# Kernel optimization log

Measured on AMD Instinct MI355X. Metric: run time of the kernel, lower is better.

Reference implementation:

```python
import jax, jax.numpy as jnp
import numpy as np

TEMPERATURE = 12.5   # init temperature
SINKHORN_EPS = 0.05  # entropic regularization replacing exact cv2.EMD LP solve
SINKHORN_ITERS = 100 # fixed iteration count (jit-friendly)


def _weight_vector(A, B):
    # A: [M,C,H,W], B: [N,C,H,W] -> [M, N, H*W]
    # matches: global-avg-pool B over HW, inner product over channels per spatial node of A
    Bp = B.mean(axis=(2, 3))                      # [N, C]
    comb = jnp.einsum('mchw,nc->mnhw', A, Bp)     # [M, N, H, W]
    comb = comb.reshape(A.shape[0], B.shape[0], -1)
    return jax.nn.relu(comb) + 0.001


def _center(x):
    # norm='center': subtract channel mean (dim 1)
    return x - x.mean(axis=1, keepdims=True)


def _similarity_map(support, query):
    # metric='cosine': sim[q, w, i, j] = cos(query[q,:,i], support[w,:,j]) over channels
    s = support.reshape(support.shape[0], support.shape[1], -1)  # [W, C, Ns]
    q = query.reshape(query.shape[0], query.shape[1], -1)        # [Q, C, Nq]
    s = s / jnp.maximum(jnp.linalg.norm(s, axis=1, keepdims=True), 1e-8)
    q = q / jnp.maximum(jnp.linalg.norm(q, axis=1, keepdims=True), 1e-8)
    return jnp.einsum('qci,wcj->qwij', q, s)                     # [Q, W, Nq, Ns]


def _sinkhorn_flow(cost, a, b, eps=SINKHORN_EPS, n_iters=SINKHORN_ITERS):
    # Batched entropic OT in log-space. cost: [..., n, m]; a: [..., n]; b: [..., m].
    log_a = jnp.log(a)
    log_b = jnp.log(b)
    logK = -cost / eps

    def body(_, uv):
        u, v = uv
        u = log_a - jax.nn.logsumexp(logK + v[..., None, :], axis=-1)
        v = log_b - jax.nn.logsumexp(logK + u[..., None], axis=-2)
        return (u, v)

    u0 = jnp.zeros_like(log_a)
    v0 = jnp.zeros_like(log_b)
    u, v = jax.lax.fori_loop(0, n_iters, body, (u0, v0))
    return jnp.exp(logK + u[..., None] + v[..., None, :])  # transport plan [..., n, m]


def setup_inputs() -> dict:
    key = jax.random.key(0)
    k1, k2 = jax.random.split(key)
    support = jax.random.normal(k1, (32, 512, 8, 8), dtype=jnp.float32)
    query = jax.random.normal(k2, (256, 512, 8, 8), dtype=jnp.float32)
    return {"support": support, "query": query}


def reference(support, query):
    # weight_1: [Q, W, N] (row/query-node marginals), weight_2: [W, Q, N] (col/support-node)
    w1 = _weight_vector(query, support)
    w2 = _weight_vector(support, query)

    s = _center(support)
    q = _center(query)
    sim = _similarity_map(s, q)  # [Q, W, N, N]

    num_node = w1.shape[-1]
    # opencv path: relu (no-op, already >0) + 1e-5, rescale so each marginal sums to num_node
    a = w1 + 1e-5
    a = a * (num_node / a.sum(-1, keepdims=True))              # [Q, W, N]
    b = jnp.transpose(w2, (1, 0, 2)) + 1e-5                    # weight_2[j, i] -> [Q, W, N]
    b = b * (num_node / b.sum(-1, keepdims=True))

    flow = _sinkhorn_flow(1.0 - sim, a, b)                     # [Q, W, N, N]
    flow = jax.lax.stop_gradient(flow)  # opencv flow is a non-differentiable constant

    logits = (sim * flow).sum((-1, -2)) * (TEMPERATURE / num_node)  # [Q, W]
    return logits
```

## Files before the change

### kernel.cpp

```cpp
#include <hip/hip_runtime.h>
#include <math.h>


#define DEV static __device__ __forceinline__

typedef _Float16 half8 __attribute__((ext_vector_type(8)));
typedef float floatx4 __attribute__((ext_vector_type(4)));

DEV float fast_rcp(float x) {
#if __has_builtin(__builtin_amdgcn_rcpf)
    return __builtin_amdgcn_rcpf(x);
#else
    return 1.0f / x;
#endif
}
DEV float fexp2(float x) {
#if __has_builtin(__builtin_amdgcn_exp2f)
    return __builtin_amdgcn_exp2f(x);
#else
    return exp2f(x);
#endif
}
DEV float flog2(float x) {
#if __has_builtin(__builtin_amdgcn_logf)
    return __builtin_amdgcn_logf(x);
#else
    return log2f(x);
#endif
}

#define K_SIM2M 28.853900817779268f
#define K_M2SIM 0.034657359027997264f
#define LDP 68
#define LDPH 72

__global__ void __launch_bounds__(1024, 1)
norm_kernel(const float* __restrict__ support, const float* __restrict__ query,
            _Float16* __restrict__ Vht, _Float16* __restrict__ Uht,
            float* __restrict__ BpT, float* __restrict__ QpT,
            float* __restrict__ muA, float* __restrict__ nrmA,
            float* __restrict__ Ssc) {
    __shared__ float red1[16][64];
    __shared__ float red2[16][64];
    __shared__ float muL[64], invL[64];
    __shared__ float tile[128][65];

    int sid = blockIdx.x;
    const float* src;
    _Float16* dst;
    float* poolT;
    int pstride, pidx;
    if (sid < 32) {
        src = support + (size_t)sid * 32768; dst = Vht + (size_t)sid * 32768;
        poolT = BpT; pstride = 32; pidx = sid;
    } else {
        src = query + (size_t)(sid - 32) * 32768; dst = Uht + (size_t)(sid - 32) * 32768;
        poolT = QpT; pstride = 256; pidx = sid - 32;
    }

    int node = threadIdx.x & 63;
    int cq   = threadIdx.x >> 6;

    float s1 = 0.f, s2 = 0.f;
#pragma unroll 8
    for (int j = 0; j < 32; ++j) {
        int c = cq * 32 + j;
        float x = src[c * 64 + node];
        s1 += x; s2 += x * x;
        float ps = x;
        ps += __shfl_xor(ps, 1);  ps += __shfl_xor(ps, 2);  ps += __shfl_xor(ps, 4);
        ps += __shfl_xor(ps, 8);  ps += __shfl_xor(ps, 16); ps += __shfl_xor(ps, 32);
        if (node == 0) poolT[(size_t)c * pstride + pidx] = ps * (1.0f / 64.0f);
    }
    red1[cq][node] = s1;
    red2[cq][node] = s2;
    __syncthreads();
    if (threadIdx.x < 64) {
        float t1 = 0.f, t2 = 0.f;
#pragma unroll
        for (int k = 0; k < 16; ++k) { t1 += red1[k][node]; t2 += red2[k][node]; }
        float mu  = t1 * (1.0f / 512.0f);
        float ss  = t2 - 512.0f * mu * mu;
        float nrm = fmaxf(sqrtf(fmaxf(ss, 0.0f)), 1e-8f);
        muL[node]  = mu;
        invL[node] = 1.0f / nrm;
        muA[sid * 64 + node]  = mu;
        nrmA[sid * 64 + node] = nrm;
        float sS = t1;
        sS += __shfl_xor(sS, 1);  sS += __shfl_xor(sS, 2);  sS += __shfl_xor(sS, 4);
        sS += __shfl_xor(sS, 8);  sS += __shfl_xor(sS, 16); sS += __shfl_xor(sS, 32);
        if (node == 0) Ssc[sid] = sS * (1.0f / 64.0f);
    }
    __syncthreads();

    float mu = muL[node], inv = invL[node];
    for (int ch = 0; ch < 4; ++ch) {
#pragma unroll
        for (int j = 0; j < 8; ++j) {
            int cl = cq * 8 + j;
            float x = src[(ch * 128 + cl) * 64 + node];
            tile[cl][node] = (x - mu) * inv;
        }
        __syncthreads();
        {
            int g    = threadIdx.x;
            int slot = g & 63;
            int t    = (g >> 6) & 3;
            int kkl  = g >> 8;
            int nd   = t * 16 + (slot & 15);
            int c8   = (kkl << 2) | (slot >> 4);
            half8 v;
#pragma unroll
            for (int i = 0; i < 8; ++i) v[i] = (_Float16)tile[c8 * 8 + i][nd];
            *(half8*)(dst + ((size_t)ch * 1024 + g) * 8) = v;
        }
        __syncthreads();
    }
}

__global__ void __launch_bounds__(256)
marg_kernel(const _Float16* __restrict__ Uht, const _Float16* __restrict__ Vht,
            const float* __restrict__ BpT, const float* __restrict__ QpT,
            const float* __restrict__ muA, const float* __restrict__ nrmA,
            const float* __restrict__ Ssc,
            float* __restrict__ a_out, float* __restrict__ b_out) {
    __shared__ __align__(16) float WL[512 * 32];
    __shared__ float Sl[32];
    int lane = threadIdx.x & 63;
    int kq   = threadIdx.x >> 6;

    const _Float16* src16;
    float mu, nrm;
    if (blockIdx.x < 256) {
        int q = (blockIdx.x & 7) * 32 + (blockIdx.x >> 3);
        for (int t = threadIdx.x; t < 4096; t += 256)
            ((float4*)WL)[t] = ((const float4*)BpT)[t];
        if (threadIdx.x < 32) Sl[threadIdx.x] = Ssc[threadIdx.x];
        src16 = Uht + (size_t)q * 32768;
        mu  = muA[(32 + q) * 64 + lane];
        nrm = nrmA[(32 + q) * 64 + lane];
    } else {
        int id = blockIdx.x - 256;
        int w = id >> 3, qg = id & 7;
        for (int t = threadIdx.x; t < 4096; t += 256) {
            int c = t >> 3, k = t & 7;
            ((float4*)WL)[t] = ((const float4*)(QpT + (size_t)c * 256 + qg * 32))[k];
        }
        if (threadIdx.x < 32) Sl[threadIdx.x] = Ssc[32 + qg * 32 + threadIdx.x];
        src16 = Vht + (size_t)w * 32768;
        mu  = muA[w * 64 + lane];
        nrm = nrmA[w * 64 + lane];
    }
    __syncthreads();

    int lbase = (lane >> 4) * 64 + (lane & 15);
    float acc[8] = {0, 0, 0, 0, 0, 0, 0, 0};
#pragma unroll 1
    for (int kk = 0; kk < 16; ++kk) {
#pragma unroll
        for (int hi = 0; hi < 4; ++hi) {
            half8 x8 = *(const half8*)(src16 +
                        ((size_t)(kk * 256 + lbase + (hi << 4)) * 8));
            int cb = kk * 32 + hi * 8;
#pragma unroll
            for (int j = 0; j < 8; ++j) {
                float xv = (float)x8[j];
                const float* wl = WL + (cb + j) * 32 + kq * 8;
                float4 b0 = *(const float4*)wl;
                float4 b1 = *(const float4*)(wl + 4);
                acc[0] = fmaf(xv, b0.x, acc[0]); acc[1] = fmaf(xv, b0.y, acc[1]);
                acc[2] = fmaf(xv, b0.z, acc[2]); acc[3] = fmaf(xv, b0.w, acc[3]);
                acc[4] = fmaf(xv, b1.x, acc[4]); acc[5] = fmaf(xv, b1.y, acc[5]);
                acc[6] = fmaf(xv, b1.z, acc[6]); acc[7] = fmaf(xv, b1.w, acc[7]);
            }
        }
    }
#pragma unroll
    for (int k = 0; k < 8; ++k) {
        float raw = fmaf(mu, Sl[kq * 8 + k], nrm * acc[k]);
        float v = fmaxf(raw, 0.0f) + 0.001f;
        v += 1e-5f;
        float s = v;
        s += __shfl_xor(s, 1);  s += __shfl_xor(s, 2);  s += __shfl_xor(s, 4);
        s += __shfl_xor(s, 8);  s += __shfl_xor(s, 16); s += __shfl_xor(s, 32);
        v = v * (64.0f / s);
        if (blockIdx.x < 256) {
            int q = (blockIdx.x & 7) * 32 + (blockIdx.x >> 3), w = kq * 8 + k;
            a_out[((size_t)q * 32 + w) * 64 + lane] = v;
        } else {
            int id = blockIdx.x - 256;
            int w = id >> 3, q = (id & 7) * 32 + kq * 8 + k;
            b_out[((size_t)w * 256 + q) * 64 + lane] = v;
        }
    }
}

__global__ void __launch_bounds__(256, 4)
emd_kernel(const _Float16* __restrict__ Uht, const _Float16* __restrict__ Vht,
           const float* __restrict__ a_arr, const float* __restrict__ b_arr,
           float* __restrict__ out) {
    __shared__ __align__(16) _Float16 T[4][64 * LDPH];

    int x    = blockIdx.x & 7;
    int i    = blockIdx.x >> 3;
    int w    = i & 31;
    int wave = threadIdx.x >> 6;
    int lane = threadIdx.x & 63;
    int q    = (x * 8 + (i >> 5)) * 4 + wave;
    int lo16 = lane & 15;
    int hi4  = lane >> 4;
    int ig   = lane >> 3;
    int jg   = lane & 7;

    floatx4 acc[4][4];
#pragma unroll
    for (int tm = 0; tm < 4; ++tm)
#pragma unroll
        for (int tn = 0; tn < 4; ++tn)
            acc[tm][tn] = (floatx4){0.f, 0.f, 0.f, 0.f};

    const _Float16* Abase = Uht + (size_t)q * 32768 + lane * 8;
    const _Float16* Bbase = Vht + (size_t)w * 32768 + lane * 8;
#pragma unroll 1
    for (int kk = 0; kk < 16; ++kk) {
        half8 bf[4];
#pragma unroll
        for (int t = 0; t < 4; ++t)
            bf[t] = *(const half8*)(Bbase + (size_t)(kk * 4 + t) * 512);
#pragma unroll
        for (int tm = 0; tm < 4; ++tm) {
            half8 af = *(const half8*)(Abase + (size_t)(kk * 4 + tm) * 512);
#pragma unroll
            for (int tn = 0; tn < 4; ++tn)
                acc[tm][tn] = __builtin_amdgcn_mfma_f32_16x16x32_f16(
                    af, bf[tn], acc[tm][tn], 0, 0, 0);
        }
    }

    float lmax = -2.0f;
#pragma unroll
    for (int tm = 0; tm < 4; ++tm)
#pragma unroll
        for (int tn = 0; tn < 4; ++tn)
#pragma unroll
            for (int r = 0; r < 4; ++r) lmax = fmaxf(lmax, acc[tm][tn][r]);
    lmax = fmaxf(lmax, __shfl_xor(lmax, 1));
    lmax = fmaxf(lmax, __shfl_xor(lmax, 2));
    lmax = fmaxf(lmax, __shfl_xor(lmax, 4));
    lmax = fmaxf(lmax, __shfl_xor(lmax, 8));
    lmax = fmaxf(lmax, __shfl_xor(lmax, 16));
    lmax = fmaxf(lmax, __shfl_xor(lmax, 32));
    float s0 = lmax;

    {
        _Float16* buf = T[wave];
#pragma unroll
        for (int tm = 0; tm < 4; ++tm)
#pragma unroll
            for (int tn = 0; tn < 4; ++tn)
#pragma unroll
                for (int r = 0; r < 4; ++r) {
                    int row = tm * 16 + hi4 * 4 + r;
                    int col = tn * 16 + lo16;
                    int sp  = (col & 7) ^ (row >> 3);
                    buf[row * LDPH + (col & ~7) + sp] =
                        (_Float16)fexp2((acc[tm][tn][r] - s0) * K_SIM2M);
                }
    }
    __syncthreads();
    float Mf[8][8];
    {
        const _Float16* buf = T[wave];
#pragma unroll
        for (int t = 0; t < 8; ++t) {
            half8 h = *(const half8*)(buf + (ig * 8 + (jg ^ t)) * LDPH + jg * 8);
#pragma unroll
            for (int c = 0; c < 8; ++c) Mf[t][c] = (float)h[c];
        }
    }

    int gp = q * 32 + w;
    float a_own = a_arr[(size_t)gp * 64 + ig * 8 + jg];
    float b_own = b_arr[((size_t)w * 256 + q) * 64 + jg * 8 + ig];

    float wvp[8];
#pragma unroll
    for (int s = 0; s < 8; ++s) wvp[s] = 1.0f;
    float q8[8];
    float w_prev = -1.f;

#pragma unroll 1
    for (int it = 0; it < 100; ++it) {
        float p[8];
#pragma unroll
        for (int t = 0; t < 8; ++t) {
            float s = Mf[t][0] * wvp[0];
#pragma unroll
            for (int c = 1; c < 8; ++c) s = fmaf(Mf[t][c], wvp[c], s);
            p[t] = s;
        }
        p[0] += __shfl_xor(p[4], 4); p[1] += __shfl_xor(p[5], 4);
        p[2] += __shfl_xor(p[6], 4); p[3] += __shfl_xor(p[7], 4);
        p[0] += __shfl_xor(p[2], 2); p[1] += __shfl_xor(p[3], 2);
        p[0] += __shfl_xor(p[1], 1);
        float z_own = a_own * fast_rcp(p[0]);
        q8[0] = z_own;
        q8[1] = __shfl_xor(q8[0], 1);
        q8[2] = __shfl_xor(q8[0], 2); q8[3] = __shfl_xor(q8[1], 2);
        q8[4] = __shfl_xor(q8[0], 4); q8[5] = __shfl_xor(q8[1], 4);
        q8[6] = __shfl_xor(q8[2], 4); q8[7] = __shfl_xor(q8[3], 4);
        float cp[8];
#pragma unroll
        for (int s = 0; s < 8; ++s) {
            float v = Mf[0][s] * q8[0];
#pragma unroll
            for (int t = 1; t < 8; ++t) v = fmaf(Mf[t][s], q8[t], v);
            cp[s] = v;
        }
        cp[0] += __shfl_xor(cp[4], 32); cp[1] += __shfl_xor(cp[5], 32);
        cp[2] += __shfl_xor(cp[6], 32); cp[3] += __shfl_xor(cp[7], 32);
        cp[0] += __shfl_xor(cp[2], 16); cp[1] += __shfl_xor(cp[3], 16);
        cp[0] += __shfl_xor(cp[1], 8);
        float w_own = b_own * fast_rcp(cp[0]);
        wvp[0] = w_own;
        wvp[1] = __shfl_xor(wvp[0], 8);
        wvp[2] = __shfl_xor(wvp[0], 16); wvp[3] = __shfl_xor(wvp[1], 16);
        wvp[4] = __shfl_xor(wvp[0], 32); wvp[5] = __shfl_xor(wvp[1], 32);
        wvp[6] = __shfl_xor(wvp[2], 32); wvp[7] = __shfl_xor(wvp[3], 32);
        bool same = fabsf(w_own - w_prev) <= 1e-5f * w_own;
        w_prev = w_own;
        if (__all(same)) break;
    }

    float s = 0.f;
#pragma unroll
    for (int t = 0; t < 8; ++t)
#pragma unroll
        for (int c = 0; c < 8; ++c) {
            float m    = fmaxf(Mf[t][c], 1e-30f);
            float sim  = fmaf(flog2(m), K_M2SIM, s0);
            float flow = q8[t] * m * wvp[c];
            s = fmaf(sim, flow, s);
        }
    s += __shfl_xor(s, 1);  s += __shfl_xor(s, 2);  s += __shfl_xor(s, 4);
    s += __shfl_xor(s, 8);  s += __shfl_xor(s, 16); s += __shfl_xor(s, 32);
    if (lane == 0) out[gp] = s * 0.1953125f;
}

extern "C" void kernel_launch(void* const* d_in, const int* in_sizes, int n_in,
                              void* d_out, int out_size, void* d_ws, size_t ws_size,
                              hipStream_t stream) {
    (void)in_sizes; (void)n_in; (void)out_size; (void)ws_size;
    const float* support = (const float*)d_in[0];
    const float* query   = (const float*)d_in[1];

    char* ws = (char*)d_ws;
    _Float16* Uht = (_Float16*)ws;
    _Float16* Vht = Uht + 8388608;
    float* BpT  = (float*)(Vht + 1048576);
    float* QpT  = BpT + 16384;
    float* aA   = QpT + 131072;
    float* bA   = aA + 524288;
    float* muA  = bA + 524288;
    float* nrmA = muA + 18432;
    float* Ssc  = nrmA + 18432;

    norm_kernel<<<288, 1024, 0, stream>>>(support, query, Vht, Uht, BpT, QpT,
                                          muA, nrmA, Ssc);
    marg_kernel<<<512, 256, 0, stream>>>(Uht, Vht, BpT, QpT, muA, nrmA, Ssc,
                                         aA, bA);
    emd_kernel<<<2048, 256, 0, stream>>>(Uht, Vht, aA, bA, (float*)d_out);
}
```

Measured before the change: 183.5 us.

## Fuse marginal weight computation into EMD kernel, drop separate marg kernel

Removes the standalone marg_kernel and computes the pooled-weight marginals inside emd_kernel. It accumulates dot products of the fp16 feature fragments already loaded for the MFMA similarity GEMM against the pooled vectors, then reduces them across lanes. The pooled arrays are stored row-major so each wave can read its own pool vector. The EMD block shrinks to 2 waves with 4096 blocks. This removes a kernel launch and the a/b round trip through global memory, at the cost of redundant FMA work per (q,w) pair and more register pressure in the main kernel.

```diff
diff --git a/kernel.cpp b/kernel.cpp
--- a/kernel.cpp
+++ b/kernel.cpp
@@ -31,13 +31,12 @@
 
 #define K_SIM2M 28.853900817779268f
 #define K_M2SIM 0.034657359027997264f
-#define LDP 68
 #define LDPH 72
 
 __global__ void __launch_bounds__(1024, 1)
 norm_kernel(const float* __restrict__ support, const float* __restrict__ query,
             _Float16* __restrict__ Vht, _Float16* __restrict__ Uht,
-            float* __restrict__ BpT, float* __restrict__ QpT,
+            float* __restrict__ Bp, float* __restrict__ Qp,
             float* __restrict__ muA, float* __restrict__ nrmA,
             float* __restrict__ Ssc) {
     __shared__ float red1[16][64];
@@ -49,13 +48,13 @@
     const float* src;
     _Float16* dst;
     float* poolT;
-    int pstride, pidx;
+    int pidx;
     if (sid < 32) {
         src = support + (size_t)sid * 32768; dst = Vht + (size_t)sid * 32768;
-        poolT = BpT; pstride = 32; pidx = sid;
+        poolT = Bp; pidx = sid;
     } else {
         src = query + (size_t)(sid - 32) * 32768; dst = Uht + (size_t)(sid - 32) * 32768;
-        poolT = QpT; pstride = 256; pidx = sid - 32;
+        poolT = Qp; pidx = sid - 32;
     }
 
     int node = threadIdx.x & 63;
@@ -70,7 +69,7 @@
         float ps = x;
         ps += __shfl_xor(ps, 1);  ps += __shfl_xor(ps, 2);  ps += __shfl_xor(ps, 4);
         ps += __shfl_xor(ps, 8);  ps += __shfl_xor(ps, 16); ps += __shfl_xor(ps, 32);
-        if (node == 0) poolT[(size_t)c * pstride + pidx] = ps * (1.0f / 64.0f);
+        if (node == 0) poolT[(size_t)pidx * 512 + c] = ps * (1.0f / 64.0f);
     }
     red1[cq][node] = s1;
     red2[cq][node] = s2;
@@ -118,95 +117,20 @@
     }
 }
 
-__global__ void __launch_bounds__(256)
-marg_kernel(const _Float16* __restrict__ Uht, const _Float16* __restrict__ Vht,
-            const float* __restrict__ BpT, const float* __restrict__ QpT,
-            const float* __restrict__ muA, const float* __restrict__ nrmA,
-            const float* __restrict__ Ssc,
-            float* __restrict__ a_out, float* __restrict__ b_out) {
-    __shared__ __align__(16) float WL[512 * 32];
-    __shared__ float Sl[32];
-    int lane = threadIdx.x & 63;
-    int kq   = threadIdx.x >> 6;
-
-    const _Float16* src16;
-    float mu, nrm;
-    if (blockIdx.x < 256) {
-        int q = (blockIdx.x & 7) * 32 + (blockIdx.x >> 3);
-        for (int t = threadIdx.x; t < 4096; t += 256)
-            ((float4*)WL)[t] = ((const float4*)BpT)[t];
-        if (threadIdx.x < 32) Sl[threadIdx.x] = Ssc[threadIdx.x];
-        src16 = Uht + (size_t)q * 32768;
-        mu  = muA[(32 + q) * 64 + lane];
-        nrm = nrmA[(32 + q) * 64 + lane];
-    } else {
-        int id = blockIdx.x - 256;
-        int w = id >> 3, qg = id & 7;
-        for (int t = threadIdx.x; t < 4096; t += 256) {
-            int c = t >> 3, k = t & 7;
-            ((float4*)WL)[t] = ((const float4*)(QpT + (size_t)c * 256 + qg * 32))[k];
-        }
-        if (threadIdx.x < 32) Sl[threadIdx.x] = Ssc[32 + qg * 32 + threadIdx.x];
-        src16 = Vht + (size_t)w * 32768;
-        mu  = muA[w * 64 + lane];
-        nrm = nrmA[w * 64 + lane];
-    }
-    __syncthreads();
-
-    int lbase = (lane >> 4) * 64 + (lane & 15);
-    float acc[8] = {0, 0, 0, 0, 0, 0, 0, 0};
-#pragma unroll 1
-    for (int kk = 0; kk < 16; ++kk) {
-#pragma unroll
-        for (int hi = 0; hi < 4; ++hi) {
-            half8 x8 = *(const half8*)(src16 +
-                        ((size_t)(kk * 256 + lbase + (hi << 4)) * 8));
-            int cb = kk * 32 + hi * 8;
-#pragma unroll
-            for (int j = 0; j < 8; ++j) {
-                float xv = (float)x8[j];
-                const float* wl = WL + (cb + j) * 32 + kq * 8;
-                float4 b0 = *(const float4*)wl;
-                float4 b1 = *(const float4*)(wl + 4);
-                acc[0] = fmaf(xv, b0.x, acc[0]); acc[1] = fmaf(xv, b0.y, acc[1]);
-                acc[2] = fmaf(xv, b0.z, acc[2]); acc[3] = fmaf(xv, b0.w, acc[3]);
-                acc[4] = fmaf(xv, b1.x, acc[4]); acc[5] = fmaf(xv, b1.y, acc[5]);
-                acc[6] = fmaf(xv, b1.z, acc[6]); acc[7] = fmaf(xv, b1.w, acc[7]);
-            }
-        }
-    }
-#pragma unroll
-    for (int k = 0; k < 8; ++k) {
-        float raw = fmaf(mu, Sl[kq * 8 + k], nrm * acc[k]);
-        float v = fmaxf(raw, 0.0f) + 0.001f;
-        v += 1e-5f;
-        float s = v;
-        s += __shfl_xor(s, 1);  s += __shfl_xor(s, 2);  s += __shfl_xor(s, 4);
-        s += __shfl_xor(s, 8);  s += __shfl_xor(s, 16); s += __shfl_xor(s, 32);
-        v = v * (64.0f / s);
-        if (blockIdx.x < 256) {
-            int q = (blockIdx.x & 7) * 32 + (blockIdx.x >> 3), w = kq * 8 + k;
-            a_out[((size_t)q * 32 + w) * 64 + lane] = v;
-        } else {
-            int id = blockIdx.x - 256;
-            int w = id >> 3, q = (id & 7) * 32 + kq * 8 + k;
-            b_out[((size_t)w * 256 + q) * 64 + lane] = v;
-        }
-    }
-}
-
-__global__ void __launch_bounds__(256, 4)
+__global__ void __launch_bounds__(128, 4)
 emd_kernel(const _Float16* __restrict__ Uht, const _Float16* __restrict__ Vht,
-           const float* __restrict__ a_arr, const float* __restrict__ b_arr,
-           float* __restrict__ out) {
-    __shared__ __align__(16) _Float16 T[4][64 * LDPH];
+           const float* __restrict__ Bp, const float* __restrict__ Qp,
+           const float* __restrict__ muA, const float* __restrict__ nrmA,
+           const float* __restrict__ Ssc, float* __restrict__ out) {
+    __shared__ __align__(16) _Float16 T[2][64 * LDPH];
+    __shared__ float dAB[2][128];
 
     int x    = blockIdx.x & 7;
     int i    = blockIdx.x >> 3;
     int w    = i & 31;
     int wave = threadIdx.x >> 6;
     int lane = threadIdx.x & 63;
-    int q    = (x * 8 + (i >> 5)) * 4 + wave;
+    int q    = x * 32 + (i >> 5) * 2 + wave;
     int lo16 = lane & 15;
     int hi4  = lane >> 4;
     int ig   = lane >> 3;
@@ -218,15 +142,32 @@
 #pragma unroll
         for (int tn = 0; tn < 4; ++tn)
             acc[tm][tn] = (floatx4){0.f, 0.f, 0.f, 0.f};
+    float accA[4] = {0.f, 0.f, 0.f, 0.f};
+    float accB[4] = {0.f, 0.f, 0.f, 0.f};
 
     const _Float16* Abase = Uht + (size_t)q * 32768 + lane * 8;
     const _Float16* Bbase = Vht + (size_t)w * 32768 + lane * 8;
+    const float* Bpw = Bp + (size_t)w * 512 + hi4 * 8;
+    const float* Qpq = Qp + (size_t)q * 512 + hi4 * 8;
 #pragma unroll 1
     for (int kk = 0; kk < 16; ++kk) {
+        float4 wb0 = *(const float4*)(Bpw + kk * 32);
+        float4 wb1 = *(const float4*)(Bpw + kk * 32 + 4);
+        float4 wq0 = *(const float4*)(Qpq + kk * 32);
+        float4 wq1 = *(const float4*)(Qpq + kk * 32 + 4);
         half8 bf[4];
 #pragma unroll
         for (int t = 0; t < 4; ++t)
             bf[t] = *(const half8*)(Bbase + (size_t)(kk * 4 + t) * 512);
+#pragma unroll
+        for (int tn = 0; tn < 4; ++tn) {
+            float s = accB[tn];
+            s = fmaf((float)bf[tn][0], wq0.x, s); s = fmaf((float)bf[tn][1], wq0.y, s);
+            s = fmaf((float)bf[tn][2], wq0.z, s); s = fmaf((float)bf[tn][3], wq0.w, s);
+            s = fmaf((float)bf[tn][4], wq1.x, s); s = fmaf((float)bf[tn][5], wq1.y, s);
+            s = fmaf((float)bf[tn][6], wq1.z, s); s = fmaf((float)bf[tn][7], wq1.w, s);
+            accB[tn] = s;
+        }
 #pragma unroll
         for (int tm = 0; tm < 4; ++tm) {
             half8 af = *(const half8*)(Abase + (size_t)(kk * 4 + tm) * 512);
@@ -234,6 +175,26 @@
             for (int tn = 0; tn < 4; ++tn)
                 acc[tm][tn] = __builtin_amdgcn_mfma_f32_16x16x32_f16(
                     af, bf[tn], acc[tm][tn], 0, 0, 0);
+            float s = accA[tm];
+            s = fmaf((float)af[0], wb0.x, s); s = fmaf((float)af[1], wb0.y, s);
+            s = fmaf((float)af[2], wb0.z, s); s = fmaf((float)af[3], wb0.w, s);
+            s = fmaf((float)af[4], wb1.x, s); s = fmaf((float)af[5], wb1.y, s);
+            s = fmaf((float)af[6], wb1.z, s); s = fmaf((float)af[7], wb1.w, s);
+            accA[tm] = s;
+        }
+    }
+
+    {
+        float* dA = dAB[wave];
+        float* dB = dAB[wave] + 64;
+#pragma unroll
+        for (int t = 0; t < 4; ++t) {
+            accA[t] += __shfl_xor(accA[t], 16);
+            accA[t] += __shfl_xor(accA[t], 32);
+            accB[t] += __shfl_xor(accB[t], 16);
+            accB[t] += __shfl_xor(accB[t], 32);
+            dA[t * 16 + lo16] = accA[t];
+            dB[t * 16 + lo16] = accB[t];
         }
     }
 
@@ -280,8 +241,30 @@
     }
 
     int gp = q * 32 + w;
-    float a_own = a_arr[(size_t)gp * 64 + ig * 8 + jg];
-    float b_own = b_arr[((size_t)w * 256 + q) * 64 + jg * 8 + ig];
+    float a_own, b_own;
+    {
+        const float* dA = dAB[wave];
+        const float* dB = dAB[wave] + 64;
+        float Sw = Ssc[w];
+        float Sq = Ssc[32 + q];
+        float muq = muA[(32 + q) * 64 + lane];
+        float nrq = nrmA[(32 + q) * 64 + lane];
+        float va = fmaxf(fmaf(muq, Sw, nrq * dA[lane]), 0.0f) + 0.001f;
+        va += 1e-5f;
+        float sa = va;
+        sa += __shfl_xor(sa, 1);  sa += __shfl_xor(sa, 2);  sa += __shfl_xor(sa, 4);
+        sa += __shfl_xor(sa, 8);  sa += __shfl_xor(sa, 16); sa += __shfl_xor(sa, 32);
+        a_own = va * (64.0f / sa);
+        int nb = ((lane & 7) << 3) | (lane >> 3);
+        float muw = muA[w * 64 + nb];
+        float nrw = nrmA[w * 64 + nb];
+        float vb = fmaxf(fmaf(muw, Sq, nrw * dB[nb]), 0.0f) + 0.001f;
+        vb += 1e-5f;
+        float sb = vb;
+        sb += __shfl_xor(sb, 1);  sb += __shfl_xor(sb, 2);  sb += __shfl_xor(sb, 4);
+        sb += __shfl_xor(sb, 8);  sb += __shfl_xor(sb, 16); sb += __shfl_xor(sb, 32);
+        b_own = vb * (64.0f / sb);
+    }
 
     float wvp[8];
 #pragma unroll
@@ -357,17 +340,14 @@
     char* ws = (char*)d_ws;
     _Float16* Uht = (_Float16*)ws;
     _Float16* Vht = Uht + 8388608;
-    float* BpT  = (float*)(Vht + 1048576);
-    float* QpT  = BpT + 16384;
-    float* aA   = QpT + 131072;
-    float* bA   = aA + 524288;
-    float* muA  = bA + 524288;
+    float* Bpp  = (float*)(Vht + 1048576);
+    float* Qpp  = Bpp + 16384;
+    float* muA  = Qpp + 131072;
     float* nrmA = muA + 18432;
     float* Ssc  = nrmA + 18432;
 
-    norm_kernel<<<288, 1024, 0, stream>>>(support, query, Vht, Uht, BpT, QpT,
+    norm_kernel<<<288, 1024, 0, stream>>>(support, query, Vht, Uht, Bpp, Qpp,
                                           muA, nrmA, Ssc);
-    marg_kernel<<<512, 256, 0, stream>>>(Uht, Vht, BpT, QpT, muA, nrmA, Ssc,
-                                         aA, bA);
-    emd_kernel<<<2048, 256, 0, stream>>>(Uht, Vht, aA, bA, (float*)d_out);
-}
+    emd_kernel<<<4096, 128, 0, stream>>>(Uht, Vht, Bpp, Qpp, muA, nrmA, Ssc,
+                                         (float*)d_out);
+}
```

Measured after the change: 188.7 us. 2.8% more time.
